# Kernel optimization log

Hardware: AMD Instinct MI355X
Metric: run time of the kernel (lower is better)

The kernel has to match this reference:

```python
import jax, jax.numpy as jnp
import numpy as np

B, N, C = 128, 197, 768
H = 12
HID = 3072
DROP = 0.1
EPS = 1e-5


def _layernorm(x, g, b):
    m = jnp.mean(x, axis=-1, keepdims=True)
    v = jnp.var(x, axis=-1, keepdims=True)
    return (x - m) * jax.lax.rsqrt(v + EPS) * g + b


def setup_inputs() -> dict:
    key = jax.random.key(0)
    ks = jax.random.split(key, 6)
    def lin(k, fan_in, fan_out):
        return (jax.random.normal(k, (fan_in, fan_out), jnp.float32) * (fan_in ** -0.5))
    return {
        "x": jax.random.normal(ks[0], (B, N, C), jnp.float32),
        "ln1_g": jnp.ones((C,), jnp.float32),
        "ln1_b": jnp.zeros((C,), jnp.float32),
        "Wqkv": lin(ks[1], C, 3 * C),          # qkv_bias=False
        "Wproj": lin(ks[2], C, C),
        "bproj": jnp.zeros((C,), jnp.float32),
        "ln2_g": jnp.ones((C,), jnp.float32),
        "ln2_b": jnp.zeros((C,), jnp.float32),
        "W1": lin(ks[3], C, HID),
        "b1": jnp.zeros((HID,), jnp.float32),
        "W2": lin(ks[4], HID, C),
        "b2": jnp.zeros((C,), jnp.float32),
    }


def reference(x, ln1_g, ln1_b, Wqkv, Wproj, bproj, ln2_g, ln2_b, W1, b1, W2, b2):
    Bx, Nx, Cx = x.shape
    hd = Cx // H
    thr = int((Nx - 1) * DROP)            # 19
    keep = (Nx - 1) - (thr + 1)           # 176 patches kept (rank > thr)

    # ---- drop_low_attn: unscaled q@k^T, mean over heads, cls->patch scores ----
    qkv = (x @ Wqkv).reshape(Bx, Nx, 3, H, hd).transpose(2, 0, 3, 1, 4)
    q, k = qkv[0], qkv[1]
    attn0 = jnp.einsum('bhnd,bhmd->bhnm', q, k)        # no scale, no softmax
    scores = jnp.mean(attn0, axis=1)[:, 0, 1:]          # [B, N-1]
    rank = jnp.argsort(jnp.argsort(scores, axis=1), axis=1)
    keep_mask = rank > thr                              # exactly `keep` True per row
    # indices of kept patches in original order (stable argsort of ~mask)
    idx = jnp.argsort((~keep_mask).astype(jnp.int32), axis=1)[:, :keep] + 1
    tok = jnp.concatenate([jnp.zeros((Bx, 1), idx.dtype), idx], axis=1)  # cls + kept
    x = jnp.take_along_axis(x, tok[:, :, None], axis=1) / (1.0 - DROP)   # [B, 177, C]
    Np = keep + 1

    # ---- attention block (scaled softmax attention) ----
    h = _layernorm(x, ln1_g, ln1_b)
    qkv2 = (h @ Wqkv).reshape(Bx, Np, 3, H, hd).transpose(2, 0, 3, 1, 4)
    q2, k2, v2 = qkv2[0], qkv2[1], qkv2[2]
    a = jax.nn.softmax(jnp.einsum('bhnd,bhmd->bhnm', q2, k2) * (hd ** -0.5), axis=-1)
    o = jnp.einsum('bhnm,bhmd->bhnd', a, v2).transpose(0, 2, 1, 3).reshape(Bx, Np, Cx)
    x = x + (o @ Wproj + bproj)

    # ---- MLP block ----
    h = _layernorm(x, ln2_g, ln2_b)
    x = x + (jax.nn.gelu(h @ W1 + b1, approximate=False) @ W2 + b2)
    return x
```

## Files before the change

### kernel.cpp

```cpp
#include <hip/hip_runtime.h>
#include <math.h>

#define BB 128
#define NTOK 197
#define CC 768
#define HH 12
#define HD 64
#define HIDN 3072
#define NP 177
#define NPATCH 196
#define THRK 19
#define MR (BB*NP)

using short8 = __attribute__((ext_vector_type(8))) short;
using f32x4  = __attribute__((ext_vector_type(4))) float;

__device__ __forceinline__ unsigned short f2b(float f){
  unsigned u = __builtin_bit_cast(unsigned, f);
  u += 0x7fffu + ((u >> 16) & 1u);
  return (unsigned short)(u >> 16);
}

__device__ __forceinline__ void gload16(const void* src, void* lds){
  __builtin_amdgcn_global_load_lds(
      (const __attribute__((address_space(1))) unsigned int*)src,
      (__attribute__((address_space(3))) unsigned int*)lds,
      16, 0, 0);
}

__global__ void tcvt_kernel(const float* __restrict__ in, unsigned short* __restrict__ out, int K, int N){
  __shared__ float tile[64][65];
  int n0 = blockIdx.x*64, k0 = blockIdx.y*64;
  int t = threadIdx.x;
  int r = t >> 6, c = t & 63;
  #pragma unroll
  for (int i = 0; i < 16; ++i)
    tile[r + i*4][c] = in[(size_t)(k0 + r + i*4)*N + n0 + c];
  __syncthreads();
  #pragma unroll
  for (int i = 0; i < 16; ++i)
    out[(size_t)(n0 + r + i*4)*K + k0 + c] = f2b(tile[c][r + i*4]);
}

__global__ void q0_kernel(const float* __restrict__ x, const float* __restrict__ Wqkv, float* __restrict__ q0){
  int b = blockIdx.x, t = threadIdx.x;
  int c = blockIdx.y*256 + t;
  __shared__ float xs[CC];
  for (int j = t; j < CC; j += 256) xs[j] = x[(size_t)b*NTOK*CC + j];
  __syncthreads();
  double acc = 0.0;
  for (int j = 0; j < CC; ++j) acc = fma((double)xs[j], (double)Wqkv[(size_t)j*(3*CC) + c], acc);
  q0[b*CC + c] = (float)acc;
}

__global__ void wvec_kernel(const float* __restrict__ Wqkv, const float* __restrict__ q0, float* __restrict__ wv){
  int b = blockIdx.x, t = threadIdx.x;
  int j = blockIdx.y*256 + t;
  __shared__ float qs[CC];
  for (int c = t; c < CC; c += 256) qs[c] = q0[b*CC + c];
  __syncthreads();
  const float* row = Wqkv + (size_t)j*(3*CC) + CC;
  double acc = 0.0;
  for (int c = 0; c < CC; ++c) acc = fma((double)row[c], (double)qs[c], acc);
  wv[b*CC + j] = (float)acc;
}

__global__ void score_kernel(const float* __restrict__ x, const float* __restrict__ wv, float* __restrict__ sc){
  int m = blockIdx.x, b = blockIdx.y, l = threadIdx.x;
  const float* xr = x + ((size_t)b*NTOK + 1 + m)*CC;
  const float* wr = wv + b*CC;
  double acc = 0.0;
  for (int c = l; c < CC; c += 64) acc = fma((double)xr[c], (double)wr[c], acc);
  for (int off = 32; off; off >>= 1) acc += __shfl_down(acc, off);
  if (l == 0) sc[b*NPATCH + m] = (float)(acc * (1.0/12.0));
}

__global__ void select_kernel(const float* __restrict__ sc, int* __restrict__ tok){
  int b = blockIdx.x, t = threadIdx.x;
  __shared__ float s[NPATCH];
  __shared__ int kp[NPATCH];
  for (int m = t; m < NPATCH; m += 256) s[m] = sc[b*NPATCH + m];
  __syncthreads();
  for (int m = t; m < NPATCH; m += 256){
    float v = s[m]; int rank = 0;
    for (int j = 0; j < NPATCH; ++j){
      float u = s[j];
      rank += (u < v) || (u == v && j < m);
    }
    kp[m] = (rank > THRK) ? 1 : 0;
  }
  __syncthreads();
  for (int m = t; m < NPATCH; m += 256){
    if (kp[m]){
      int pos = 0;
      for (int j = 0; j < m; ++j) pos += kp[j];
      tok[b*NP + 1 + pos] = m + 1;
    }
  }
  if (t == 0) tok[b*NP] = 0;
}

__global__ void gather_kernel(const float* __restrict__ x, const int* __restrict__ tok, float* __restrict__ xk){
  int i = blockIdx.x, b = blockIdx.y, t = threadIdx.x;
  int src = tok[b*NP + i];
  const float* xr = x + ((size_t)b*NTOK + src)*CC;
  float* o = xk + ((size_t)b*NP + i)*CC;
  for (int c = t; c < CC; c += 256) o[c] = xr[c] * (1.0f/0.9f);
}

__global__ void ln_kernel(const float* __restrict__ in, const float* __restrict__ g,
                          const float* __restrict__ bt, unsigned short* __restrict__ out){
  int row = blockIdx.x, t = threadIdx.x;
  const float* xr = in + (size_t)row*CC;
  float v0 = xr[t], v1 = xr[t+256], v2 = xr[t+512];
  float s = v0+v1+v2, ss = v0*v0+v1*v1+v2*v2;
  for (int off = 32; off; off >>= 1){ s += __shfl_down(s, off); ss += __shfl_down(ss, off); }
  __shared__ float red[8];
  int wid = t >> 6, lane = t & 63;
  if (lane == 0){ red[wid] = s; red[4+wid] = ss; }
  __syncthreads();
  if (t == 0){
    float S = red[0]+red[1]+red[2]+red[3], SS = red[4]+red[5]+red[6]+red[7];
    float mean = S * (1.0f/CC);
    float var = SS * (1.0f/CC) - mean*mean;
    red[0] = mean; red[1] = rsqrtf(var + 1e-5f);
  }
  __syncthreads();
  float mean = red[0], rstd = red[1];
  unsigned short* orow = out + (size_t)row*CC;
  orow[t]     = f2b((v0-mean)*rstd*g[t]     + bt[t]);
  orow[t+256] = f2b((v1-mean)*rstd*g[t+256] + bt[t+256]);
  orow[t+512] = f2b((v2-mean)*rstd*g[t+512] + bt[t+512]);
}

template<int EPI>
__global__ __launch_bounds__(256) void gemm128(
    const unsigned short* __restrict__ A, const unsigned short* __restrict__ Bt,
    const float* __restrict__ bias, const float* __restrict__ res, void* __restrict__ outp,
    int M, int N, int K)
{
  __shared__ __align__(16) short As[2][128*32];
  __shared__ __align__(16) short Bs[2][128*32];
  int nwg = gridDim.x, o = blockIdx.x;
  int q = nwg >> 3, rr = nwg & 7;
  int xcd = o & 7, seq = o >> 3;
  int wg = (xcd < rr) ? xcd*(q+1) + seq : rr*(q+1) + (xcd - rr)*q + seq;
  int nx = N >> 7;
  int m0 = (wg / nx) << 7, n0 = (wg % nx) << 7;

  int t = threadIdx.x, w = t >> 6, l = t & 63;
  int wr = w >> 1, wc = w & 1;
  int srow = w*16 + (l >> 2);
  int sk8  = (l & 3)*8;
  const unsigned short* Abase = A  + (size_t)(m0 + srow)*K + sk8;
  const unsigned short* Bbase = Bt + (size_t)(n0 + srow)*K + sk8;
  f32x4 acc[4][4] = {};

  int nt = K >> 5;
  #pragma unroll
  for (int j = 0; j < 2; ++j){
    gload16(Abase + (size_t)(j*64)*K, &As[0][(j*64 + w*16)*32]);
    gload16(Bbase + (size_t)(j*64)*K, &Bs[0][(j*64 + w*16)*32]);
  }
  __syncthreads();

  int cur = 0;
  for (int ti = 0; ti < nt; ++ti){
    if (ti + 1 < nt){
      int kt = (ti + 1) << 5;
      #pragma unroll
      for (int j = 0; j < 2; ++j){
        gload16(Abase + (size_t)(j*64)*K + kt, &As[cur^1][(j*64 + w*16)*32]);
        gload16(Bbase + (size_t)(j*64)*K + kt, &Bs[cur^1][(j*64 + w*16)*32]);
      }
    }
    short8 af[4], bf[4];
    #pragma unroll
    for (int i = 0; i < 4; ++i){
      af[i] = *reinterpret_cast<const short8*>(&As[cur][(wr*64 + i*16 + (l&15))*32 + (l>>4)*8]);
      bf[i] = *reinterpret_cast<const short8*>(&Bs[cur][(wc*64 + i*16 + (l&15))*32 + (l>>4)*8]);
    }
    #pragma unroll
    for (int i = 0; i < 4; ++i)
      #pragma unroll
      for (int jn = 0; jn < 4; ++jn)
        acc[i][jn] = __builtin_amdgcn_mfma_f32_16x16x32_bf16(af[i], bf[jn], acc[i][jn], 0, 0, 0);
    __syncthreads();
    cur ^= 1;
  }

  #pragma unroll
  for (int i = 0; i < 4; ++i)
  #pragma unroll
  for (int jn = 0; jn < 4; ++jn){
    int row = m0 + wr*64 + i*16 + (l>>4)*4;
    int col = n0 + wc*64 + jn*16 + (l&15);
    #pragma unroll
    for (int r = 0; r < 4; ++r){
      float v = acc[i][jn][r];
      if (EPI != 0) v += bias[col];
      if (EPI == 2) v = 0.5f*v*(1.0f + erff(v*0.70710678118f));
      if (EPI == 1 || EPI == 3) v += res[(size_t)(row+r)*N + col];
      if (EPI == 0 || EPI == 2) ((unsigned short*)outp)[(size_t)(row+r)*N + col] = f2b(v);
      else                      ((float*)outp)[(size_t)(row+r)*N + col] = v;
    }
  }
}

__global__ __launch_bounds__(256) void attn_kernel(const unsigned short* __restrict__ qkv2,
                                                   unsigned short* __restrict__ o)
{
  int rt = blockIdx.x, h = blockIdx.y, b = blockIdx.z;
  int t = threadIdx.x, w = t >> 6, l = t & 63;
  __shared__ short Vt[64*192];
  __shared__ short P[4][16*192];
  for (int idx = t; idx < NP*8; idx += 256){
    int m = idx >> 3, d0 = (idx & 7)*8;
    short8 v = *reinterpret_cast<const short8*>(qkv2 + (size_t)(b*NP+m)*(3*CC) + 2*CC + h*HD + d0);
    #pragma unroll
    for (int j = 0; j < 8; ++j) Vt[(d0+j)*192 + m] = v[j];
  }
  for (int idx = t; idx < 64*15; idx += 256){
    int d = idx/15, m = NP + idx%15;
    Vt[d*192 + m] = 0;
  }
  __syncthreads();
  int nb = rt*64 + w*16;
  int g = l >> 4, c = l & 15;
  int nq = nb + c; if (nq > NP-1) nq = NP-1;
  const unsigned short* qrow = qkv2 + (size_t)(b*NP+nq)*(3*CC) + h*HD + 8*g;
  short8 aq0 = *reinterpret_cast<const short8*>(qrow);
  short8 aq1 = *reinterpret_cast<const short8*>(qrow + 32);
  f32x4 acc[12];
  #pragma unroll
  for (int ct = 0; ct < 12; ++ct){
    int m = ct*16 + c; if (m > NP-1) m = NP-1;
    const unsigned short* krow = qkv2 + (size_t)(b*NP+m)*(3*CC) + CC + h*HD + 8*g;
    short8 bk0 = *reinterpret_cast<const short8*>(krow);
    short8 bk1 = *reinterpret_cast<const short8*>(krow + 32);
    f32x4 a = {};
    a = __builtin_amdgcn_mfma_f32_16x16x32_bf16(aq0, bk0, a, 0, 0, 0);
    a = __builtin_amdgcn_mfma_f32_16x16x32_bf16(aq1, bk1, a, 0, 0, 0);
    acc[ct] = a;
  }
  float mx[4] = {-INFINITY, -INFINITY, -INFINITY, -INFINITY};
  #pragma unroll
  for (int ct = 0; ct < 12; ++ct){
    bool valid = (ct*16 + c) < NP;
    #pragma unroll
    for (int r = 0; r < 4; ++r){
      float v = valid ? acc[ct][r]*0.125f : -INFINITY;
      acc[ct][r] = v;
      mx[r] = fmaxf(mx[r], v);
    }
  }
  #pragma unroll
  for (int off = 1; off < 16; off <<= 1){
    #pragma unroll
    for (int r = 0; r < 4; ++r) mx[r] = fmaxf(mx[r], __shfl_xor(mx[r], off));
  }
  float sm[4] = {0.f, 0.f, 0.f, 0.f};
  #pragma unroll
  for (int ct = 0; ct < 12; ++ct)
    #pragma unroll
    for (int r = 0; r < 4; ++r){
      float e = __expf(acc[ct][r] - mx[r]);
      acc[ct][r] = e; sm[r] += e;
    }
  #pragma unroll
  for (int off = 1; off < 16; off <<= 1){
    #pragma unroll
    for (int r = 0; r < 4; ++r) sm[r] += __shfl_xor(sm[r], off);
  }
  float inv[4];
  #pragma unroll
  for (int r = 0; r < 4; ++r) inv[r] = 1.0f / sm[r];
  #pragma unroll
  for (int ct = 0; ct < 12; ++ct)
    #pragma unroll
    for (int r = 0; r < 4; ++r)
      P[w][(4*g + r)*192 + ct*16 + c] = (short)f2b(acc[ct][r]*inv[r]);
  f32x4 acc2[4] = {};
  #pragma unroll
  for (int ks = 0; ks < 6; ++ks){
    short8 pa = *reinterpret_cast<const short8*>(&P[w][c*192 + ks*32 + 8*g]);
    #pragma unroll
    for (int ct2 = 0; ct2 < 4; ++ct2){
      short8 bv = *reinterpret_cast<const short8*>(&Vt[(ct2*16 + c)*192 + ks*32 + 8*g]);
      acc2[ct2] = __builtin_amdgcn_mfma_f32_16x16x32_bf16(pa, bv, acc2[ct2], 0, 0, 0);
    }
  }
  #pragma unroll
  for (int ct2 = 0; ct2 < 4; ++ct2){
    #pragma unroll
    for (int r = 0; r < 4; ++r){
      int n = nb + 4*g + r;
      if (n < NP) o[(size_t)(b*NP+n)*CC + h*HD + ct2*16 + c] = f2b(acc2[ct2][r]);
    }
  }
}

extern "C" void kernel_launch(void* const* d_in, const int* in_sizes, int n_in,
                              void* d_out, int out_size, void* d_ws, size_t ws_size,
                              hipStream_t stream) {
  const float* x     = (const float*)d_in[0];
  const float* ln1g  = (const float*)d_in[1];
  const float* ln1b  = (const float*)d_in[2];
  const float* Wqkv  = (const float*)d_in[3];
  const float* Wproj = (const float*)d_in[4];
  const float* bproj = (const float*)d_in[5];
  const float* ln2g  = (const float*)d_in[6];
  const float* ln2b  = (const float*)d_in[7];
  const float* W1    = (const float*)d_in[8];
  const float* b1    = (const float*)d_in[9];
  const float* W2    = (const float*)d_in[10];
  const float* b2    = (const float*)d_in[11];
  float* out = (float*)d_out;

  unsigned char* base = (unsigned char*)d_ws;
  size_t off = 0;
  auto alloc = [&](size_t bytes) -> void* {
    off = (off + 255) & ~(size_t)255;
    void* p = base + off;
    off += bytes;
    return p;
  };
  unsigned short* WqkvT  = (unsigned short*)alloc((size_t)(3*CC)*CC*2);
  unsigned short* WprojT = (unsigned short*)alloc((size_t)CC*CC*2);
  unsigned short* W1T    = (unsigned short*)alloc((size_t)HIDN*CC*2);
  unsigned short* W2T    = (unsigned short*)alloc((size_t)CC*HIDN*2);
  float* q0   = (float*)alloc((size_t)BB*CC*4);
  float* wv   = (float*)alloc((size_t)BB*CC*4);
  float* sc   = (float*)alloc((size_t)BB*NPATCH*4);
  int*   tok  = (int*)alloc((size_t)BB*NP*4);
  unsigned short* hbuf = (unsigned short*)alloc((size_t)MR*CC*2);
  float* xk   = (float*)alloc((size_t)MR*CC*4);
  unsigned short* qkv2 = (unsigned short*)alloc((size_t)MR*3*CC*2);
  if (off > ws_size) return;

  unsigned short* obuf = hbuf;
  unsigned short* mid  = (unsigned short*)xk;
  float* x2 = out;

  tcvt_kernel<<<dim3((3*CC)/64, CC/64), 256, 0, stream>>>(Wqkv,  WqkvT,  CC, 3*CC);
  tcvt_kernel<<<dim3(CC/64, CC/64),     256, 0, stream>>>(Wproj, WprojT, CC, CC);
  tcvt_kernel<<<dim3(HIDN/64, CC/64),   256, 0, stream>>>(W1,    W1T,    CC, HIDN);
  tcvt_kernel<<<dim3(CC/64, HIDN/64),   256, 0, stream>>>(W2,    W2T,    HIDN, CC);

  q0_kernel<<<dim3(BB, 3), 256, 0, stream>>>(x, Wqkv, q0);
  wvec_kernel<<<dim3(BB, 3), 256, 0, stream>>>(Wqkv, q0, wv);
  score_kernel<<<dim3(NPATCH, BB), 64, 0, stream>>>(x, wv, sc);
  select_kernel<<<BB, 256, 0, stream>>>(sc, tok);
  gather_kernel<<<dim3(NP, BB), 256, 0, stream>>>(x, tok, xk);

  ln_kernel<<<MR, 256, 0, stream>>>(xk, ln1g, ln1b, hbuf);
  gemm128<0><<<(MR/128)*((3*CC)/128), 256, 0, stream>>>(hbuf, WqkvT, nullptr, nullptr, qkv2, MR, 3*CC, CC);
  attn_kernel<<<dim3(3, HH, BB), 256, 0, stream>>>(qkv2, obuf);
  gemm128<1><<<(MR/128)*(CC/128), 256, 0, stream>>>(obuf, WprojT, bproj, xk, x2, MR, CC, CC);

  ln_kernel<<<MR, 256, 0, stream>>>(x2, ln2g, ln2b, hbuf);
  gemm128<2><<<(MR/128)*(HIDN/128), 256, 0, stream>>>(hbuf, W1T, b1, nullptr, mid, MR, HIDN, CC);
  gemm128<3><<<(MR/128)*(CC/128), 256, 0, stream>>>(mid, W2T, b2, x2, out, MR, CC, HIDN);
}
```

Before: 846.0 us.

## Specialise GEMM shapes, unroll double-buffer loop, fast GELU, wave-parallel wvec

Several independent changes. The GEMM takes N and K as compile-time template parameters, and its double-buffered K loop is restructured into two unrolled halves with fixed buffer indices. The exact erff in the GELU epilogue is replaced with an Abramowitz-Stegun polynomial approximation. The wvec kernel now assigns one wave per output with a shuffle reduction, giving many more blocks and coalesced row reads. The attention kernel raises wave priority around its PV MFMA loop. The polynomial GELU has error near 1e-7 and could shift outputs slightly.

```diff
diff --git a/kernel.cpp b/kernel.cpp
--- a/kernel.cpp
+++ b/kernel.cpp
@@ -21,6 +21,20 @@
   return (unsigned short)(u >> 16);
 }
 
+__device__ __forceinline__ float fast_gelu(float v){
+  float u = v * 0.70710678118654752f;
+  float a = fabsf(u);
+  float t = 1.0f / fmaf(0.3275911f, a, 1.0f);
+  float p = fmaf(1.061405429f, t, -1.453152027f);
+  p = fmaf(p, t, 1.421413741f);
+  p = fmaf(p, t, -0.284496736f);
+  p = fmaf(p, t, 0.254829592f);
+  p = p * t;
+  float e = __expf(-a*a);
+  float erfu = copysignf(1.0f - p*e, u);
+  return 0.5f * v * (1.0f + erfu);
+}
+
 __device__ __forceinline__ void gload16(const void* src, void* lds){
   __builtin_amdgcn_global_load_lds(
       (const __attribute__((address_space(1))) unsigned int*)src,
@@ -54,15 +68,15 @@
 }
 
 __global__ void wvec_kernel(const float* __restrict__ Wqkv, const float* __restrict__ q0, float* __restrict__ wv){
-  int b = blockIdx.x, t = threadIdx.x;
-  int j = blockIdx.y*256 + t;
-  __shared__ float qs[CC];
-  for (int c = t; c < CC; c += 256) qs[c] = q0[b*CC + c];
-  __syncthreads();
+  int b = blockIdx.x;
+  int j = blockIdx.y*4 + (threadIdx.x >> 6);
+  int l = threadIdx.x & 63;
   const float* row = Wqkv + (size_t)j*(3*CC) + CC;
+  const float* qs = q0 + b*CC;
   double acc = 0.0;
-  for (int c = 0; c < CC; ++c) acc = fma((double)row[c], (double)qs[c], acc);
-  wv[b*CC + j] = (float)acc;
+  for (int c = l; c < CC; c += 64) acc = fma((double)row[c], (double)qs[c], acc);
+  for (int off = 32; off; off >>= 1) acc += __shfl_down(acc, off);
+  if (l == 0) wv[b*CC + j] = (float)acc;
 }
 
 __global__ void score_kernel(const float* __restrict__ x, const float* __restrict__ wv, float* __restrict__ sc){
@@ -133,11 +147,10 @@
   orow[t+512] = f2b((v2-mean)*rstd*g[t+512] + bt[t+512]);
 }
 
-template<int EPI>
+template<int EPI, int N, int K>
 __global__ __launch_bounds__(256) void gemm128(
     const unsigned short* __restrict__ A, const unsigned short* __restrict__ Bt,
-    const float* __restrict__ bias, const float* __restrict__ res, void* __restrict__ outp,
-    int M, int N, int K)
+    const float* __restrict__ bias, const float* __restrict__ res, void* __restrict__ outp)
 {
   __shared__ __align__(16) short As[2][128*32];
   __shared__ __align__(16) short Bs[2][128*32];
@@ -145,7 +158,7 @@
   int q = nwg >> 3, rr = nwg & 7;
   int xcd = o & 7, seq = o >> 3;
   int wg = (xcd < rr) ? xcd*(q+1) + seq : rr*(q+1) + (xcd - rr)*q + seq;
-  int nx = N >> 7;
+  constexpr int nx = N >> 7;
   int m0 = (wg / nx) << 7, n0 = (wg % nx) << 7;
 
   int t = threadIdx.x, w = t >> 6, l = t & 63;
@@ -156,37 +169,38 @@
   const unsigned short* Bbase = Bt + (size_t)(n0 + srow)*K + sk8;
   f32x4 acc[4][4] = {};
 
-  int nt = K >> 5;
-  #pragma unroll
-  for (int j = 0; j < 2; ++j){
-    gload16(Abase + (size_t)(j*64)*K, &As[0][(j*64 + w*16)*32]);
-    gload16(Bbase + (size_t)(j*64)*K, &Bs[0][(j*64 + w*16)*32]);
-  }
-  __syncthreads();
-
-  int cur = 0;
-  for (int ti = 0; ti < nt; ++ti){
-    if (ti + 1 < nt){
-      int kt = (ti + 1) << 5;
-      #pragma unroll
-      for (int j = 0; j < 2; ++j){
-        gload16(Abase + (size_t)(j*64)*K + kt, &As[cur^1][(j*64 + w*16)*32]);
-        gload16(Bbase + (size_t)(j*64)*K + kt, &Bs[cur^1][(j*64 + w*16)*32]);
-      }
-    }
+  auto stage = [&](int kt, int pb){
+    #pragma unroll
+    for (int j = 0; j < 2; ++j){
+      gload16(Abase + (size_t)(j*64)*K + kt, &As[pb][(j*64 + w*16)*32]);
+      gload16(Bbase + (size_t)(j*64)*K + kt, &Bs[pb][(j*64 + w*16)*32]);
+    }
+  };
+  auto compute = [&](int pb){
     short8 af[4], bf[4];
     #pragma unroll
     for (int i = 0; i < 4; ++i){
-      af[i] = *reinterpret_cast<const short8*>(&As[cur][(wr*64 + i*16 + (l&15))*32 + (l>>4)*8]);
-      bf[i] = *reinterpret_cast<const short8*>(&Bs[cur][(wc*64 + i*16 + (l&15))*32 + (l>>4)*8]);
+      af[i] = *reinterpret_cast<const short8*>(&As[pb][(wr*64 + i*16 + (l&15))*32 + (l>>4)*8]);
+      bf[i] = *reinterpret_cast<const short8*>(&Bs[pb][(wc*64 + i*16 + (l&15))*32 + (l>>4)*8]);
     }
     #pragma unroll
     for (int i = 0; i < 4; ++i)
       #pragma unroll
       for (int jn = 0; jn < 4; ++jn)
         acc[i][jn] = __builtin_amdgcn_mfma_f32_16x16x32_bf16(af[i], bf[jn], acc[i][jn], 0, 0, 0);
+  };
+
+  constexpr int nt = K >> 5;
+  stage(0, 0);
+  __syncthreads();
+  #pragma unroll 1
+  for (int ti = 0; ti < nt; ti += 2){
+    stage((ti+1) << 5, 1);
+    compute(0);
     __syncthreads();
-    cur ^= 1;
+    if (ti + 2 < nt) stage((ti+2) << 5, 0);
+    compute(1);
+    __syncthreads();
   }
 
   #pragma unroll
@@ -199,7 +213,7 @@
     for (int r = 0; r < 4; ++r){
       float v = acc[i][jn][r];
       if (EPI != 0) v += bias[col];
-      if (EPI == 2) v = 0.5f*v*(1.0f + erff(v*0.70710678118f));
+      if (EPI == 2) v = fast_gelu(v);
       if (EPI == 1 || EPI == 3) v += res[(size_t)(row+r)*N + col];
       if (EPI == 0 || EPI == 2) ((unsigned short*)outp)[(size_t)(row+r)*N + col] = f2b(v);
       else                      ((float*)outp)[(size_t)(row+r)*N + col] = v;
@@ -281,6 +295,7 @@
     for (int r = 0; r < 4; ++r)
       P[w][(4*g + r)*192 + ct*16 + c] = (short)f2b(acc[ct][r]*inv[r]);
   f32x4 acc2[4] = {};
+  __builtin_amdgcn_s_setprio(1);
   #pragma unroll
   for (int ks = 0; ks < 6; ++ks){
     short8 pa = *reinterpret_cast<const short8*>(&P[w][c*192 + ks*32 + 8*g]);
@@ -290,6 +305,7 @@
       acc2[ct2] = __builtin_amdgcn_mfma_f32_16x16x32_bf16(pa, bv, acc2[ct2], 0, 0, 0);
     }
   }
+  __builtin_amdgcn_s_setprio(0);
   #pragma unroll
   for (int ct2 = 0; ct2 < 4; ++ct2){
     #pragma unroll
@@ -348,17 +364,17 @@
   tcvt_kernel<<<dim3(CC/64, HIDN/64),   256, 0, stream>>>(W2,    W2T,    HIDN, CC);
 
   q0_kernel<<<dim3(BB, 3), 256, 0, stream>>>(x, Wqkv, q0);
-  wvec_kernel<<<dim3(BB, 3), 256, 0, stream>>>(Wqkv, q0, wv);
+  wvec_kernel<<<dim3(BB, CC/4), 256, 0, stream>>>(Wqkv, q0, wv);
   score_kernel<<<dim3(NPATCH, BB), 64, 0, stream>>>(x, wv, sc);
   select_kernel<<<BB, 256, 0, stream>>>(sc, tok);
   gather_kernel<<<dim3(NP, BB), 256, 0, stream>>>(x, tok, xk);
 
   ln_kernel<<<MR, 256, 0, stream>>>(xk, ln1g, ln1b, hbuf);
-  gemm128<0><<<(MR/128)*((3*CC)/128), 256, 0, stream>>>(hbuf, WqkvT, nullptr, nullptr, qkv2, MR, 3*CC, CC);
+  gemm128<0, 3*CC, CC><<<(MR/128)*((3*CC)/128), 256, 0, stream>>>(hbuf, WqkvT, nullptr, nullptr, qkv2);
   attn_kernel<<<dim3(3, HH, BB), 256, 0, stream>>>(qkv2, obuf);
-  gemm128<1><<<(MR/128)*(CC/128), 256, 0, stream>>>(obuf, WprojT, bproj, xk, x2, MR, CC, CC);
+  gemm128<1, CC, CC><<<(MR/128)*(CC/128), 256, 0, stream>>>(obuf, WprojT, bproj, xk, x2);
 
   ln_kernel<<<MR, 256, 0, stream>>>(x2, ln2g, ln2b, hbuf);
-  gemm128<2><<<(MR/128)*(HIDN/128), 256, 0, stream>>>(hbuf, W1T, b1, nullptr, mid, MR, HIDN, CC);
-  gemm128<3><<<(MR/128)*(CC/128), 256, 0, stream>>>(mid, W2T, b2, x2, out, MR, CC, HIDN);
-}
+  gemm128<2, HIDN, CC><<<(MR/128)*(HIDN/128), 256, 0, stream>>>(hbuf, W1T, b1, nullptr, mid);
+  gemm128<3, CC, HIDN><<<(MR/128)*(CC/128), 256, 0, stream>>>(mid, W2T, b2, x2, out);
+}
```

Result: slower. 913.1 us (+7.9%).

## Stage bf16 GEMM epilogue through LDS, use fast GELU, parallelize wvec

Applied to the files above, without the earlier changes.

The bf16-output GEMM epilogues now write each wave's tile into reused shared memory and then issue coalesced 16-byte row stores, replacing scattered 2-byte writes. The exact erff GELU is replaced with a polynomial erf approximation (Abramowitz-Stegun 7.1.26) to cut transcendental cost in the W1 epilogue. wvec_kernel changes from a serial per-thread dot product with strided row loads to one wavefront per output with coalesced loads and a shuffle reduction. A priority hint is added around the PV MFMA loop in attention. The GELU approximation carries a small accuracy risk.

```diff
diff --git a/kernel.cpp b/kernel.cpp
--- a/kernel.cpp
+++ b/kernel.cpp
@@ -21,6 +21,20 @@
   return (unsigned short)(u >> 16);
 }
 
+__device__ __forceinline__ float fast_gelu(float v){
+  float u = v * 0.70710678118654752f;
+  float a = fabsf(u);
+  float t = 1.0f / fmaf(0.3275911f, a, 1.0f);
+  float p = fmaf(1.061405429f, t, -1.453152027f);
+  p = fmaf(p, t, 1.421413741f);
+  p = fmaf(p, t, -0.284496736f);
+  p = fmaf(p, t, 0.254829592f);
+  p = p * t;
+  float e = __expf(-a*a);
+  float erfu = copysignf(1.0f - p*e, u);
+  return 0.5f * v * (1.0f + erfu);
+}
+
 __device__ __forceinline__ void gload16(const void* src, void* lds){
   __builtin_amdgcn_global_load_lds(
       (const __attribute__((address_space(1))) unsigned int*)src,
@@ -54,15 +68,15 @@
 }
 
 __global__ void wvec_kernel(const float* __restrict__ Wqkv, const float* __restrict__ q0, float* __restrict__ wv){
-  int b = blockIdx.x, t = threadIdx.x;
-  int j = blockIdx.y*256 + t;
-  __shared__ float qs[CC];
-  for (int c = t; c < CC; c += 256) qs[c] = q0[b*CC + c];
-  __syncthreads();
+  int b = blockIdx.x;
+  int j = blockIdx.y*4 + (threadIdx.x >> 6);
+  int l = threadIdx.x & 63;
   const float* row = Wqkv + (size_t)j*(3*CC) + CC;
+  const float* qs = q0 + b*CC;
   double acc = 0.0;
-  for (int c = 0; c < CC; ++c) acc = fma((double)row[c], (double)qs[c], acc);
-  wv[b*CC + j] = (float)acc;
+  for (int c = l; c < CC; c += 64) acc = fma((double)row[c], (double)qs[c], acc);
+  for (int off = 32; off; off >>= 1) acc += __shfl_down(acc, off);
+  if (l == 0) wv[b*CC + j] = (float)acc;
 }
 
 __global__ void score_kernel(const float* __restrict__ x, const float* __restrict__ wv, float* __restrict__ sc){
@@ -139,8 +153,7 @@
     const float* __restrict__ bias, const float* __restrict__ res, void* __restrict__ outp,
     int M, int N, int K)
 {
-  __shared__ __align__(16) short As[2][128*32];
-  __shared__ __align__(16) short Bs[2][128*32];
+  __shared__ __align__(16) short sm[4*128*32];
   int nwg = gridDim.x, o = blockIdx.x;
   int q = nwg >> 3, rr = nwg & 7;
   int xcd = o & 7, seq = o >> 3;
@@ -159,8 +172,8 @@
   int nt = K >> 5;
   #pragma unroll
   for (int j = 0; j < 2; ++j){
-    gload16(Abase + (size_t)(j*64)*K, &As[0][(j*64 + w*16)*32]);
-    gload16(Bbase + (size_t)(j*64)*K, &Bs[0][(j*64 + w*16)*32]);
+    gload16(Abase + (size_t)(j*64)*K, &sm[(j*64 + w*16)*32]);
+    gload16(Bbase + (size_t)(j*64)*K, &sm[8192 + (j*64 + w*16)*32]);
   }
   __syncthreads();
 
@@ -170,15 +183,15 @@
       int kt = (ti + 1) << 5;
       #pragma unroll
       for (int j = 0; j < 2; ++j){
-        gload16(Abase + (size_t)(j*64)*K + kt, &As[cur^1][(j*64 + w*16)*32]);
-        gload16(Bbase + (size_t)(j*64)*K + kt, &Bs[cur^1][(j*64 + w*16)*32]);
+        gload16(Abase + (size_t)(j*64)*K + kt, &sm[(cur^1)*4096 + (j*64 + w*16)*32]);
+        gload16(Bbase + (size_t)(j*64)*K + kt, &sm[8192 + (cur^1)*4096 + (j*64 + w*16)*32]);
       }
     }
     short8 af[4], bf[4];
     #pragma unroll
     for (int i = 0; i < 4; ++i){
-      af[i] = *reinterpret_cast<const short8*>(&As[cur][(wr*64 + i*16 + (l&15))*32 + (l>>4)*8]);
-      bf[i] = *reinterpret_cast<const short8*>(&Bs[cur][(wc*64 + i*16 + (l&15))*32 + (l>>4)*8]);
+      af[i] = *reinterpret_cast<const short8*>(&sm[cur*4096 + (wr*64 + i*16 + (l&15))*32 + (l>>4)*8]);
+      bf[i] = *reinterpret_cast<const short8*>(&sm[8192 + cur*4096 + (wc*64 + i*16 + (l&15))*32 + (l>>4)*8]);
     }
     #pragma unroll
     for (int i = 0; i < 4; ++i)
@@ -189,20 +202,44 @@
     cur ^= 1;
   }
 
-  #pragma unroll
-  for (int i = 0; i < 4; ++i)
-  #pragma unroll
-  for (int jn = 0; jn < 4; ++jn){
-    int row = m0 + wr*64 + i*16 + (l>>4)*4;
-    int col = n0 + wc*64 + jn*16 + (l&15);
-    #pragma unroll
-    for (int r = 0; r < 4; ++r){
-      float v = acc[i][jn][r];
-      if (EPI != 0) v += bias[col];
-      if (EPI == 2) v = 0.5f*v*(1.0f + erff(v*0.70710678118f));
-      if (EPI == 1 || EPI == 3) v += res[(size_t)(row+r)*N + col];
-      if (EPI == 0 || EPI == 2) ((unsigned short*)outp)[(size_t)(row+r)*N + col] = f2b(v);
-      else                      ((float*)outp)[(size_t)(row+r)*N + col] = v;
+  if (EPI == 0 || EPI == 2){
+    short* my = &sm[w*4096];
+    #pragma unroll
+    for (int i = 0; i < 4; ++i)
+    #pragma unroll
+    for (int jn = 0; jn < 4; ++jn){
+      int lr0 = i*16 + (l>>4)*4;
+      int lc  = jn*16 + (l&15);
+      int col = n0 + wc*64 + lc;
+      #pragma unroll
+      for (int r = 0; r < 4; ++r){
+        float v = acc[i][jn][r];
+        if (EPI == 2) { v += bias[col]; v = fast_gelu(v); }
+        my[(lr0 + r)*64 + lc] = (short)f2b(v);
+      }
+    }
+    __syncthreads();
+    unsigned short* ob = (unsigned short*)outp;
+    #pragma unroll
+    for (int p = 0; p < 8; ++p){
+      int idx = p*512 + l*8;
+      int rr2 = idx >> 6, cc2 = idx & 63;
+      short8 vv = *reinterpret_cast<const short8*>(&my[idx]);
+      *reinterpret_cast<short8*>(ob + (size_t)(m0 + wr*64 + rr2)*N + n0 + wc*64 + cc2) = vv;
+    }
+  } else {
+    #pragma unroll
+    for (int i = 0; i < 4; ++i)
+    #pragma unroll
+    for (int jn = 0; jn < 4; ++jn){
+      int row = m0 + wr*64 + i*16 + (l>>4)*4;
+      int col = n0 + wc*64 + jn*16 + (l&15);
+      #pragma unroll
+      for (int r = 0; r < 4; ++r){
+        float v = acc[i][jn][r] + bias[col];
+        v += res[(size_t)(row+r)*N + col];
+        ((float*)outp)[(size_t)(row+r)*N + col] = v;
+      }
     }
   }
 }
@@ -259,28 +296,29 @@
     #pragma unroll
     for (int r = 0; r < 4; ++r) mx[r] = fmaxf(mx[r], __shfl_xor(mx[r], off));
   }
-  float sm[4] = {0.f, 0.f, 0.f, 0.f};
+  float sm2[4] = {0.f, 0.f, 0.f, 0.f};
   #pragma unroll
   for (int ct = 0; ct < 12; ++ct)
     #pragma unroll
     for (int r = 0; r < 4; ++r){
       float e = __expf(acc[ct][r] - mx[r]);
-      acc[ct][r] = e; sm[r] += e;
+      acc[ct][r] = e; sm2[r] += e;
     }
   #pragma unroll
   for (int off = 1; off < 16; off <<= 1){
     #pragma unroll
-    for (int r = 0; r < 4; ++r) sm[r] += __shfl_xor(sm[r], off);
+    for (int r = 0; r < 4; ++r) sm2[r] += __shfl_xor(sm2[r], off);
   }
   float inv[4];
   #pragma unroll
-  for (int r = 0; r < 4; ++r) inv[r] = 1.0f / sm[r];
+  for (int r = 0; r < 4; ++r) inv[r] = 1.0f / sm2[r];
   #pragma unroll
   for (int ct = 0; ct < 12; ++ct)
     #pragma unroll
     for (int r = 0; r < 4; ++r)
       P[w][(4*g + r)*192 + ct*16 + c] = (short)f2b(acc[ct][r]*inv[r]);
   f32x4 acc2[4] = {};
+  __builtin_amdgcn_s_setprio(1);
   #pragma unroll
   for (int ks = 0; ks < 6; ++ks){
     short8 pa = *reinterpret_cast<const short8*>(&P[w][c*192 + ks*32 + 8*g]);
@@ -290,6 +328,7 @@
       acc2[ct2] = __builtin_amdgcn_mfma_f32_16x16x32_bf16(pa, bv, acc2[ct2], 0, 0, 0);
     }
   }
+  __builtin_amdgcn_s_setprio(0);
   #pragma unroll
   for (int ct2 = 0; ct2 < 4; ++ct2){
     #pragma unroll
@@ -348,7 +387,7 @@
   tcvt_kernel<<<dim3(CC/64, HIDN/64),   256, 0, stream>>>(W2,    W2T,    HIDN, CC);
 
   q0_kernel<<<dim3(BB, 3), 256, 0, stream>>>(x, Wqkv, q0);
-  wvec_kernel<<<dim3(BB, 3), 256, 0, stream>>>(Wqkv, q0, wv);
+  wvec_kernel<<<dim3(BB, CC/4), 256, 0, stream>>>(Wqkv, q0, wv);
   score_kernel<<<dim3(NPATCH, BB), 64, 0, stream>>>(x, wv, sc);
   select_kernel<<<BB, 256, 0, stream>>>(sc, tok);
   gather_kernel<<<dim3(NP, BB), 256, 0, stream>>>(x, tok, xk);
```

Measured after the change: 855.9 us. No clear change (+1.2%).

## Parallelize wvec reduction across wavefronts, use polynomial GELU, raise MFMA priority

Applied to the files above, without the earlier changes.

The wvec kernel now assigns one wavefront per output element. Each wavefront reads its Wqkv row with coalesced strided loads and finishes with a shuffle reduction, replacing the old scheme of one thread looping serially over a whole row with uncoalesced access. The GELU epilogue in the MLP GEMM swaps erff for an Abramowitz-Stegun polynomial approximation built on __expf, which is cheaper but slightly less accurate. The attention kernel raises wave priority around the P·V MFMA loop. It also renames a local variable.

```diff
diff --git a/kernel.cpp b/kernel.cpp
--- a/kernel.cpp
+++ b/kernel.cpp
@@ -21,6 +21,20 @@
   return (unsigned short)(u >> 16);
 }
 
+__device__ __forceinline__ float fast_gelu(float v){
+  float u = v * 0.70710678118654752f;
+  float a = fabsf(u);
+  float t = 1.0f / fmaf(0.3275911f, a, 1.0f);
+  float p = fmaf(1.061405429f, t, -1.453152027f);
+  p = fmaf(p, t, 1.421413741f);
+  p = fmaf(p, t, -0.284496736f);
+  p = fmaf(p, t, 0.254829592f);
+  p = p * t;
+  float e = __expf(-a*a);
+  float erfu = copysignf(1.0f - p*e, u);
+  return 0.5f * v * (1.0f + erfu);
+}
+
 __device__ __forceinline__ void gload16(const void* src, void* lds){
   __builtin_amdgcn_global_load_lds(
       (const __attribute__((address_space(1))) unsigned int*)src,
@@ -54,15 +68,15 @@
 }
 
 __global__ void wvec_kernel(const float* __restrict__ Wqkv, const float* __restrict__ q0, float* __restrict__ wv){
-  int b = blockIdx.x, t = threadIdx.x;
-  int j = blockIdx.y*256 + t;
-  __shared__ float qs[CC];
-  for (int c = t; c < CC; c += 256) qs[c] = q0[b*CC + c];
-  __syncthreads();
+  int b = blockIdx.x;
+  int j = blockIdx.y*4 + (threadIdx.x >> 6);
+  int l = threadIdx.x & 63;
   const float* row = Wqkv + (size_t)j*(3*CC) + CC;
+  const float* qs = q0 + b*CC;
   double acc = 0.0;
-  for (int c = 0; c < CC; ++c) acc = fma((double)row[c], (double)qs[c], acc);
-  wv[b*CC + j] = (float)acc;
+  for (int c = l; c < CC; c += 64) acc = fma((double)row[c], (double)qs[c], acc);
+  for (int off = 32; off; off >>= 1) acc += __shfl_down(acc, off);
+  if (l == 0) wv[b*CC + j] = (float)acc;
 }
 
 __global__ void score_kernel(const float* __restrict__ x, const float* __restrict__ wv, float* __restrict__ sc){
@@ -199,7 +213,7 @@
     for (int r = 0; r < 4; ++r){
       float v = acc[i][jn][r];
       if (EPI != 0) v += bias[col];
-      if (EPI == 2) v = 0.5f*v*(1.0f + erff(v*0.70710678118f));
+      if (EPI == 2) v = fast_gelu(v);
       if (EPI == 1 || EPI == 3) v += res[(size_t)(row+r)*N + col];
       if (EPI == 0 || EPI == 2) ((unsigned short*)outp)[(size_t)(row+r)*N + col] = f2b(v);
       else                      ((float*)outp)[(size_t)(row+r)*N + col] = v;
@@ -259,28 +273,29 @@
     #pragma unroll
     for (int r = 0; r < 4; ++r) mx[r] = fmaxf(mx[r], __shfl_xor(mx[r], off));
   }
-  float sm[4] = {0.f, 0.f, 0.f, 0.f};
+  float sm2[4] = {0.f, 0.f, 0.f, 0.f};
   #pragma unroll
   for (int ct = 0; ct < 12; ++ct)
     #pragma unroll
     for (int r = 0; r < 4; ++r){
       float e = __expf(acc[ct][r] - mx[r]);
-      acc[ct][r] = e; sm[r] += e;
+      acc[ct][r] = e; sm2[r] += e;
     }
   #pragma unroll
   for (int off = 1; off < 16; off <<= 1){
     #pragma unroll
-    for (int r = 0; r < 4; ++r) sm[r] += __shfl_xor(sm[r], off);
+    for (int r = 0; r < 4; ++r) sm2[r] += __shfl_xor(sm2[r], off);
   }
   float inv[4];
   #pragma unroll
-  for (int r = 0; r < 4; ++r) inv[r] = 1.0f / sm[r];
+  for (int r = 0; r < 4; ++r) inv[r] = 1.0f / sm2[r];
   #pragma unroll
   for (int ct = 0; ct < 12; ++ct)
     #pragma unroll
     for (int r = 0; r < 4; ++r)
       P[w][(4*g + r)*192 + ct*16 + c] = (short)f2b(acc[ct][r]*inv[r]);
   f32x4 acc2[4] = {};
+  __builtin_amdgcn_s_setprio(1);
   #pragma unroll
   for (int ks = 0; ks < 6; ++ks){
     short8 pa = *reinterpret_cast<const short8*>(&P[w][c*192 + ks*32 + 8*g]);
@@ -290,6 +305,7 @@
       acc2[ct2] = __builtin_amdgcn_mfma_f32_16x16x32_bf16(pa, bv, acc2[ct2], 0, 0, 0);
     }
   }
+  __builtin_amdgcn_s_setprio(0);
   #pragma unroll
   for (int ct2 = 0; ct2 < 4; ++ct2){
     #pragma unroll
@@ -348,7 +364,7 @@
   tcvt_kernel<<<dim3(CC/64, HIDN/64),   256, 0, stream>>>(W2,    W2T,    HIDN, CC);
 
   q0_kernel<<<dim3(BB, 3), 256, 0, stream>>>(x, Wqkv, q0);
-  wvec_kernel<<<dim3(BB, 3), 256, 0, stream>>>(Wqkv, q0, wv);
+  wvec_kernel<<<dim3(BB, CC/4), 256, 0, stream>>>(Wqkv, q0, wv);
   score_kernel<<<dim3(NPATCH, BB), 64, 0, stream>>>(x, wv, sc);
   select_kernel<<<BB, 256, 0, stream>>>(sc, tok);
   gather_kernel<<<dim3(NP, BB), 256, 0, stream>>>(x, tok, xk);
```

After: 844.1 us. No clear change (-0.2%).
